# Performance work log

Hardware: AMD Instinct MI355X
Metric: run time of the kernel (lower is better)

## Reference

```python
import jax, jax.numpy as jnp
import numpy as np

N, C, H, W = 128, 3, 256, 256
MAXNORM = 5.371920351148152
MAX_SQ = 16  # static bound for data-dependent squaring loop
PADE_B = [6.476475253248e+16, 3.238237626624e+16, 7771770303897600.0,
          1187353796428800.0, 129060195264000.0, 10559470521600.0,
          670442572800.0, 33522128640.0, 1323241920.0, 40840800.0,
          960960.0, 16380.0, 182.0, 1.0]


def pade13(A):
    b = PADE_B
    I = jnp.eye(A.shape[-1], dtype=A.dtype)
    A2 = A @ A
    A4 = A2 @ A2
    A6 = A4 @ A2
    U = A @ (A6 @ (b[13] * A6 + b[11] * A4 + b[9] * A2)
             + b[7] * A6 + b[5] * A4 + b[3] * A2 + b[1] * I)
    V = (A6 @ (b[12] * A6 + b[10] * A4 + b[8] * A2)
         + b[6] * A6 + b[4] * A4 + b[2] * A2 + b[0] * I)
    return U, V


def expm_affine(theta):  # theta: [N,2,3] -> exp of padded 3x3, top 2 rows
    n = theta.shape[0]
    A = jnp.concatenate([theta, jnp.zeros((n, 1, 3), theta.dtype)], axis=1)
    fro = jnp.sqrt(jnp.sum(A * A, axis=(1, 2), keepdims=True))
    n_sq = jnp.maximum(0.0, jnp.ceil(jnp.log2(fro / MAXNORM)))
    Asc = A / (2.0 ** n_sq)
    U, V = pade13(Asc)
    R = jnp.linalg.solve(U + V, -U + V)
    k = n_sq.reshape(n).astype(jnp.int32)
    def body(i, Rc):
        return jnp.where((i < k)[:, None, None], jnp.matmul(Rc, Rc), Rc)
    R = jax.lax.fori_loop(0, MAX_SQ, body, R)
    return R[:, :2, :]


def affine_grid(theta, Ho, Wo):  # align_corners=True
    xs = jnp.linspace(-1.0, 1.0, Wo, dtype=theta.dtype)
    ys = jnp.linspace(-1.0, 1.0, Ho, dtype=theta.dtype)
    gy, gx = jnp.meshgrid(ys, xs, indexing='ij')          # [Ho,Wo]
    base = jnp.stack([gx, gy, jnp.ones_like(gx)], axis=-1)  # [Ho,Wo,3]
    return jnp.einsum('hwk,nck->nhwc', base, theta)        # [N,Ho,Wo,2]


def grid_sample(x, grid):  # bilinear, zeros padding, align_corners=True
    _, _, Hi, Wi = x.shape
    ix = (grid[..., 0] + 1.0) * 0.5 * (Wi - 1)
    iy = (grid[..., 1] + 1.0) * 0.5 * (Hi - 1)
    ix0 = jnp.floor(ix)
    iy0 = jnp.floor(iy)
    ix1 = ix0 + 1.0
    iy1 = iy0 + 1.0
    wx1 = ix - ix0; wx0 = 1.0 - wx1
    wy1 = iy - iy0; wy0 = 1.0 - wy1

    def gather(yy, xx):
        valid = ((yy >= 0) & (yy < Hi) & (xx >= 0) & (xx < Wi))
        yc = jnp.clip(yy, 0, Hi - 1).astype(jnp.int32)
        xc = jnp.clip(xx, 0, Wi - 1).astype(jnp.int32)
        vals = jax.vmap(lambda img, y, xi: img[:, y, xi])(x, yc, xc)  # [N,C,Ho,Wo]
        return vals * valid[:, None].astype(x.dtype)

    return (gather(iy0, ix0) * (wy0 * wx0)[:, None]
            + gather(iy0, ix1) * (wy0 * wx1)[:, None]
            + gather(iy1, ix0) * (wy1 * wx0)[:, None]
            + gather(iy1, ix1) * (wy1 * wx1)[:, None])


def setup_inputs() -> dict:
    key = jax.random.key(0)
    k1, k2 = jax.random.split(key)
    x = jax.random.normal(k1, (N, C, H, W), dtype=jnp.float32)
    theta = 0.1 * jax.random.normal(k2, (N, 6), dtype=jnp.float32)
    return {"x": x, "theta": theta}


def reference(x, theta):
    th = expm_affine(theta.reshape(-1, 2, 3))  # [N,2,3]
    grid = affine_grid(th, H, W)               # [N,H,W,2]
    return grid_sample(x, grid)                # [N,C,H,W]
```

## Files before the change

### kernel.cpp

```cpp
#include <hip/hip_runtime.h>

#define Ndim 128
#define Cdim 3
#define Hdim 256
#define Wdim 256
#define HW (Hdim * Wdim)
#define MAXNORM_F 5.371920351148152f

#define LCOLS 56
#define LROWS 48
#define LBUF  (LCOLS * LROWS)

typedef float vf2 __attribute__((ext_vector_type(2)));
typedef unsigned int uint32;

__device__ __forceinline__ void mm3f(const float a[3][3], const float b[3][3], float c[3][3]) {
    #pragma unroll
    for (int i = 0; i < 3; ++i)
        #pragma unroll
        for (int j = 0; j < 3; ++j) {
            float s = 0.0f;
            #pragma unroll
            for (int k = 0; k < 3; ++k) s = fmaf(a[i][k], b[k][j], s);
            c[i][j] = s;
        }
}

__global__ void expm_kernel(const float* __restrict__ theta, float* __restrict__ thOut) {
    int n = blockIdx.x * blockDim.x + threadIdx.x;
    if (n >= Ndim) return;

    const float b[14] = {6.476475253248e+16f, 3.238237626624e+16f, 7771770303897600.0f,
                         1187353796428800.0f, 129060195264000.0f, 10559470521600.0f,
                         670442572800.0f, 33522128640.0f, 1323241920.0f, 40840800.0f,
                         960960.0f, 16380.0f, 182.0f, 1.0f};

    float A[3][3];
    #pragma unroll
    for (int j = 0; j < 3; ++j) {
        A[0][j] = theta[n * 6 + j];
        A[1][j] = theta[n * 6 + 3 + j];
        A[2][j] = 0.0f;
    }

    float fro2 = 0.0f;
    #pragma unroll
    for (int i = 0; i < 3; ++i)
        #pragma unroll
        for (int j = 0; j < 3; ++j) fro2 = fmaf(A[i][j], A[i][j], fro2);
    float fro = sqrtf(fro2);

    float nsq = fmaxf(0.0f, ceilf(log2f(fro / MAXNORM_F)));
    int k = (int)nsq;
    float sc = exp2f(-nsq);
    #pragma unroll
    for (int i = 0; i < 3; ++i)
        #pragma unroll
        for (int j = 0; j < 3; ++j) A[i][j] *= sc;

    float A2[3][3], A4[3][3], A6[3][3], P[3][3], Wm[3][3], T[3][3], U[3][3], V[3][3];
    mm3f(A, A, A2);
    mm3f(A2, A2, A4);
    mm3f(A4, A2, A6);

    #pragma unroll
    for (int i = 0; i < 3; ++i)
        #pragma unroll
        for (int j = 0; j < 3; ++j)
            P[i][j] = b[13] * A6[i][j] + b[11] * A4[i][j] + b[9] * A2[i][j];
    mm3f(A6, P, T);
    #pragma unroll
    for (int i = 0; i < 3; ++i)
        #pragma unroll
        for (int j = 0; j < 3; ++j)
            Wm[i][j] = T[i][j] + b[7] * A6[i][j] + b[5] * A4[i][j] + b[3] * A2[i][j]
                       + (i == j ? b[1] : 0.0f);
    mm3f(A, Wm, U);

    #pragma unroll
    for (int i = 0; i < 3; ++i)
        #pragma unroll
        for (int j = 0; j < 3; ++j)
            P[i][j] = b[12] * A6[i][j] + b[10] * A4[i][j] + b[8] * A2[i][j];
    mm3f(A6, P, T);
    #pragma unroll
    for (int i = 0; i < 3; ++i)
        #pragma unroll
        for (int j = 0; j < 3; ++j)
            V[i][j] = T[i][j] + b[6] * A6[i][j] + b[4] * A4[i][j] + b[2] * A2[i][j]
                      + (i == j ? b[0] : 0.0f);

    float M[3][6];
    #pragma unroll
    for (int i = 0; i < 3; ++i)
        #pragma unroll
        for (int j = 0; j < 3; ++j) {
            M[i][j]     = U[i][j] + V[i][j];
            M[i][j + 3] = V[i][j] - U[i][j];
        }
    #pragma unroll
    for (int col = 0; col < 3; ++col) {
        int piv = col;
        float best = fabsf(M[col][col]);
        for (int r = col + 1; r < 3; ++r) {
            float v = fabsf(M[r][col]);
            if (v > best) { best = v; piv = r; }
        }
        if (piv != col) {
            #pragma unroll
            for (int j = 0; j < 6; ++j) {
                float t = M[col][j]; M[col][j] = M[piv][j]; M[piv][j] = t;
            }
        }
        float inv = 1.0f / M[col][col];
        #pragma unroll
        for (int j = 0; j < 6; ++j) M[col][j] *= inv;
        #pragma unroll
        for (int r = 0; r < 3; ++r) {
            if (r == col) continue;
            float f = M[r][col];
            #pragma unroll
            for (int j = 0; j < 6; ++j) M[r][j] -= f * M[col][j];
        }
    }
    float R[3][3];
    #pragma unroll
    for (int i = 0; i < 3; ++i)
        #pragma unroll
        for (int j = 0; j < 3; ++j) R[i][j] = M[i][j + 3];

    for (int i = 0; i < 16; ++i) {
        if (i < k) {
            float Rn[3][3];
            mm3f(R, R, Rn);
            #pragma unroll
            for (int a = 0; a < 3; ++a)
                #pragma unroll
                for (int c = 0; c < 3; ++c) R[a][c] = Rn[a][c];
        }
    }

    #pragma unroll
    for (int j = 0; j < 3; ++j) {
        thOut[n * 6 + j]     = (float)R[0][j];
        thOut[n * 6 + 3 + j] = (float)R[1][j];
    }
}

__global__ __launch_bounds__(256) void sample_kernel(const float* __restrict__ x,
                                                     const float* __restrict__ th,
                                                     float* __restrict__ out) {
    __shared__ float lds[2][LBUF];

    const int nwg_per_xcd = 8192 / 8;
    int bid = blockIdx.x;
    int wgid = (bid & 7) * nwg_per_xcd + (bid >> 3);

    int tw  = wgid & 7;
    int thp = (wgid >> 3) & 7;
    int n   = wgid >> 6;

    int tid = threadIdx.x;
    int w  = (tw << 5) + (tid & 31);
    int h0 = (thp << 5) + ((tid >> 5) << 2);

    const float* t = th + n * 6;
    float t0 = t[0], t1 = t[1], t2 = t[2], t3 = t[3], t4 = t[4], t5 = t[5];

    float Cx = 127.5f * (t2 - t0 - t1 + 1.0f);
    float Cy = 127.5f * (t5 - t3 - t4 + 1.0f);

    float fwA = (float)(tw << 5),  fwB = fwA + 31.0f;
    float fhA = (float)(thp << 5), fhB = fhA + 31.0f;
    float xlo = fminf(fwA * t0, fwB * t0) + fminf(fhA * t1, fhB * t1) + Cx;
    float xhi = fmaxf(fwA * t0, fwB * t0) + fmaxf(fhA * t1, fhB * t1) + Cx;
    float ylo = fminf(fwA * t3, fwB * t3) + fminf(fhA * t4, fhB * t4) + Cy;
    float yhi = fmaxf(fwA * t3, fwB * t3) + fmaxf(fhA * t4, fhB * t4) + Cy;
    int Xlo = (int)floorf(xlo) - 1, Xhi = (int)floorf(xhi) + 2;
    int Ylo = (int)floorf(ylo) - 1, Yhi = (int)floorf(yhi) + 2;
    int cn = Xhi - Xlo + 1;
    int rn = Yhi - Ylo + 1;

    size_t nbase = (size_t)n * Cdim * HW;

    float ixs[4], iys[4];
    float ixb = fmaf((float)w, t0, fmaf((float)h0, t1, Cx));
    float iyb = fmaf((float)w, t3, fmaf((float)h0, t4, Cy));
    #pragma unroll
    for (int p = 0; p < 4; ++p) {
        ixs[p] = fmaf((float)p, t1, ixb);
        iys[p] = fmaf((float)p, t4, iyb);
    }

    bool fast = (cn <= 52) && (rn <= LROWS) && (rn >= 1) && (cn >= 1);

    if (fast) {
        int bxw = (min(max(Xlo, 0), Wdim - LCOLS)) & ~3;
        int byw = min(max(Ylo, 0), Hdim - rn);
        int totc = 14 * rn;
        const float* gbase = x + nbase;

        auto stage = [&](int ch, int buf) {
            #pragma unroll
            for (int it = 0; it < 3; ++it) {
                int k = (it << 8) + tid;
                if (k < totc) {
                    int row = k / 14;
                    int col = k - row * 14;
                    const float* gp = gbase + (size_t)ch * HW
                                    + ((byw + row) << 8) + bxw + (col << 2);
                    __builtin_amdgcn_global_load_lds(
                        (const __attribute__((address_space(1))) uint32*)gp,
                        (__attribute__((address_space(3))) uint32*)
                            ((uint32*)&lds[buf][0] + ((size_t)k << 2)),
                        16, 0, 0);
                }
            }
        };

        bool interior = (Xlo >= 0) && (Xhi <= Wdim - 1) && (Ylo >= 0) && (Yhi <= Hdim - 1);

        stage(0, 0);

        int   basev[4];
        float wx1v[4], wy1v[4];
        if (interior) {
            #pragma unroll
            for (int p = 0; p < 4; ++p) {
                float ix = ixs[p], iy = iys[p];
                float fx = floorf(ix), fy = floorf(iy);
                wx1v[p] = ix - fx;
                wy1v[p] = iy - fy;
                basev[p] = ((int)fy - byw) * LCOLS + ((int)fx - bxw);
            }
        }
        size_t p0 = (size_t)h0 * Wdim + w;

        auto sample_interior = [&](int buf, int c) {
            float* o = out + nbase + (size_t)c * HW + p0;
            #pragma unroll
            for (int p = 0; p < 4; ++p) {
                const float* bp = &lds[buf][basev[p]];
                float v00 = bp[0],     v01 = bp[1];
                float v10 = bp[LCOLS], v11 = bp[LCOLS + 1];
                float wx1 = wx1v[p], wx0 = 1.0f - wx1;
                float wy1 = wy1v[p], wy0 = 1.0f - wy1;
                float top = fmaf(v01, wx1, v00 * wx0);
                float bot = fmaf(v11, wx1, v10 * wx0);
                __builtin_nontemporal_store(fmaf(wy1, bot, wy0 * top),
                                            o + (size_t)p * Wdim);
            }
        };

        auto sample_edge = [&](int buf, int c) {
            float* o = out + nbase + (size_t)c * HW + p0;
            #pragma unroll
            for (int p = 0; p < 4; ++p) {
                float ix = ixs[p], iy = iys[p];
                float fx = floorf(ix), fy = floorf(iy);
                int x0i = (int)fx, y0i = (int)fy;
                float wx1 = ix - fx, wx0 = 1.0f - wx1;
                float wy1 = iy - fy, wy0 = 1.0f - wy1;
                float mx0 = ((unsigned)x0i       < (unsigned)Wdim) ? 1.0f : 0.0f;
                float mx1 = ((unsigned)(x0i + 1) < (unsigned)Wdim) ? 1.0f : 0.0f;
                float my0 = ((unsigned)y0i       < (unsigned)Hdim) ? 1.0f : 0.0f;
                float my1 = ((unsigned)(y0i + 1) < (unsigned)Hdim) ? 1.0f : 0.0f;
                float wxm0 = wx0 * mx0, wxm1 = wx1 * mx1;
                float wym0 = wy0 * my0, wym1 = wy1 * my1;

                int lx0 = min(max(x0i - bxw, 0), LCOLS - 1);
                int lx1 = min(max(x0i + 1 - bxw, 0), LCOLS - 1);
                int ly0 = min(max(y0i - byw, 0), rn - 1);
                int ly1 = min(max(y0i + 1 - byw, 0), rn - 1);
                const float* B = &lds[buf][0];
                float v00 = B[ly0 * LCOLS + lx0], v01 = B[ly0 * LCOLS + lx1];
                float v10 = B[ly1 * LCOLS + lx0], v11 = B[ly1 * LCOLS + lx1];
                float top = fmaf(v01, wxm1, v00 * wxm0);
                float bot = fmaf(v11, wxm1, v10 * wxm0);
                __builtin_nontemporal_store(fmaf(wym1, bot, wym0 * top),
                                            o + (size_t)p * Wdim);
            }
        };

        __syncthreads();
        stage(1, 1);
        if (interior) sample_interior(0, 0); else sample_edge(0, 0);
        __syncthreads();
        stage(2, 0);
        if (interior) sample_interior(1, 1); else sample_edge(1, 1);
        __syncthreads();
        if (interior) sample_interior(0, 2); else sample_edge(0, 2);
    } else {
        const float* img0 = x + nbase;
        #pragma unroll
        for (int p = 0; p < 4; ++p) {
            float ix = ixs[p], iy = iys[p];
            float fx = floorf(ix), fy = floorf(iy);
            int ix0 = (int)fx, iy0 = (int)fy;
            float wx1 = ix - fx, wx0 = 1.0f - wx1;
            float wy1 = iy - fy, wy0 = 1.0f - wy1;
            float mx0 = ((unsigned)ix0       < (unsigned)Wdim) ? 1.0f : 0.0f;
            float mx1 = ((unsigned)(ix0 + 1) < (unsigned)Wdim) ? 1.0f : 0.0f;
            float my0 = ((unsigned)iy0       < (unsigned)Hdim) ? 1.0f : 0.0f;
            float my1 = ((unsigned)(iy0 + 1) < (unsigned)Hdim) ? 1.0f : 0.0f;
            int xc0 = min(max(ix0, 0), Wdim - 1);
            int xc1 = min(max(ix0 + 1, 0), Wdim - 1);
            int yc0 = min(max(iy0, 0), Hdim - 1);
            int yc1 = min(max(iy0 + 1, 0), Hdim - 1);
            float w00 = wy0 * wx0 * my0 * mx0;
            float w01 = wy0 * wx1 * my0 * mx1;
            float w10 = wy1 * wx0 * my1 * mx0;
            float w11 = wy1 * wx1 * my1 * mx1;
            int o00 = yc0 * Wdim + xc0, o01 = yc0 * Wdim + xc1;
            int o10 = yc1 * Wdim + xc0, o11 = yc1 * Wdim + xc1;
            #pragma unroll
            for (int c = 0; c < Cdim; ++c) {
                const float* img = img0 + (size_t)c * HW;
                float r = fmaf(img[o00], w00, fmaf(img[o01], w01,
                          fmaf(img[o10], w10, img[o11] * w11)));
                out[nbase + (size_t)c * HW + (size_t)(h0 + p) * Wdim + w] = r;
            }
        }
    }
}

extern "C" void kernel_launch(void* const* d_in, const int* in_sizes, int n_in,
                              void* d_out, int out_size, void* d_ws, size_t ws_size,
                              hipStream_t stream) {
    const float* x     = (const float*)d_in[0];
    const float* theta = (const float*)d_in[1];
    float* out = (float*)d_out;
    float* th  = (float*)d_ws;

    expm_kernel<<<1, 128, 0, stream>>>(theta, th);

    int nblocks = 8192;
    sample_kernel<<<nblocks, 256, 0, stream>>>(x, th, out);
}
```

Baseline: 41.30 us.

## Fuse matrix exponential into sampling kernel, drop separate expm launch

Removes the separate single-block expm kernel and has thread 0 of every sampling workgroup compute the 3x3 Pade matrix exponential for its batch item, sharing the result through LDS after a barrier. This eliminates one kernel launch and the dependency gap between the two kernels. In exchange, each of the 8192 workgroups redundantly runs the serial expm on one thread while the other threads wait at the barrier. It also precomputes the 1-minus interpolation weights once per pixel instead of once per channel.

```diff
diff --git a/kernel.cpp b/kernel.cpp
--- a/kernel.cpp
+++ b/kernel.cpp
@@ -26,10 +26,7 @@
         }
 }
 
-__global__ void expm_kernel(const float* __restrict__ theta, float* __restrict__ thOut) {
-    int n = blockIdx.x * blockDim.x + threadIdx.x;
-    if (n >= Ndim) return;
-
+__device__ void expm_affine_1thread(const float* __restrict__ theta, float* __restrict__ outR) {
     const float b[14] = {6.476475253248e+16f, 3.238237626624e+16f, 7771770303897600.0f,
                          1187353796428800.0f, 129060195264000.0f, 10559470521600.0f,
                          670442572800.0f, 33522128640.0f, 1323241920.0f, 40840800.0f,
@@ -38,8 +35,8 @@
     float A[3][3];
     #pragma unroll
     for (int j = 0; j < 3; ++j) {
-        A[0][j] = theta[n * 6 + j];
-        A[1][j] = theta[n * 6 + 3 + j];
+        A[0][j] = theta[j];
+        A[1][j] = theta[3 + j];
         A[2][j] = 0.0f;
     }
 
@@ -129,28 +126,27 @@
         #pragma unroll
         for (int j = 0; j < 3; ++j) R[i][j] = M[i][j + 3];
 
-    for (int i = 0; i < 16; ++i) {
-        if (i < k) {
-            float Rn[3][3];
-            mm3f(R, R, Rn);
-            #pragma unroll
-            for (int a = 0; a < 3; ++a)
-                #pragma unroll
-                for (int c = 0; c < 3; ++c) R[a][c] = Rn[a][c];
-        }
+    for (int i = 0; i < k; ++i) {
+        float Rn[3][3];
+        mm3f(R, R, Rn);
+        #pragma unroll
+        for (int a = 0; a < 3; ++a)
+            #pragma unroll
+            for (int c = 0; c < 3; ++c) R[a][c] = Rn[a][c];
     }
 
     #pragma unroll
     for (int j = 0; j < 3; ++j) {
-        thOut[n * 6 + j]     = (float)R[0][j];
-        thOut[n * 6 + 3 + j] = (float)R[1][j];
+        outR[j]     = R[0][j];
+        outR[3 + j] = R[1][j];
     }
 }
 
 __global__ __launch_bounds__(256) void sample_kernel(const float* __restrict__ x,
-                                                     const float* __restrict__ th,
+                                                     const float* __restrict__ theta,
                                                      float* __restrict__ out) {
     __shared__ float lds[2][LBUF];
+    __shared__ float thS[6];
 
     const int nwg_per_xcd = 8192 / 8;
     int bid = blockIdx.x;
@@ -164,8 +160,10 @@
     int w  = (tw << 5) + (tid & 31);
     int h0 = (thp << 5) + ((tid >> 5) << 2);
 
-    const float* t = th + n * 6;
-    float t0 = t[0], t1 = t[1], t2 = t[2], t3 = t[3], t4 = t[4], t5 = t[5];
+    if (tid == 0) expm_affine_1thread(theta + n * 6, thS);
+    __syncthreads();
+
+    float t0 = thS[0], t1 = thS[1], t2 = thS[2], t3 = thS[3], t4 = thS[4], t5 = thS[5];
 
     float Cx = 127.5f * (t2 - t0 - t1 + 1.0f);
     float Cy = 127.5f * (t5 - t3 - t4 + 1.0f);
@@ -223,14 +221,14 @@
         stage(0, 0);
 
         int   basev[4];
-        float wx1v[4], wy1v[4];
+        float wx1v[4], wx0v[4], wy1v[4], wy0v[4];
         if (interior) {
             #pragma unroll
             for (int p = 0; p < 4; ++p) {
                 float ix = ixs[p], iy = iys[p];
                 float fx = floorf(ix), fy = floorf(iy);
-                wx1v[p] = ix - fx;
-                wy1v[p] = iy - fy;
+                wx1v[p] = ix - fx; wx0v[p] = 1.0f - wx1v[p];
+                wy1v[p] = iy - fy; wy0v[p] = 1.0f - wy1v[p];
                 basev[p] = ((int)fy - byw) * LCOLS + ((int)fx - bxw);
             }
         }
@@ -243,11 +241,9 @@
                 const float* bp = &lds[buf][basev[p]];
                 float v00 = bp[0],     v01 = bp[1];
                 float v10 = bp[LCOLS], v11 = bp[LCOLS + 1];
-                float wx1 = wx1v[p], wx0 = 1.0f - wx1;
-                float wy1 = wy1v[p], wy0 = 1.0f - wy1;
-                float top = fmaf(v01, wx1, v00 * wx0);
-                float bot = fmaf(v11, wx1, v10 * wx0);
-                __builtin_nontemporal_store(fmaf(wy1, bot, wy0 * top),
+                float top = fmaf(v01, wx1v[p], v00 * wx0v[p]);
+                float bot = fmaf(v11, wx1v[p], v10 * wx0v[p]);
+                __builtin_nontemporal_store(fmaf(wy1v[p], bot, wy0v[p] * top),
                                             o + (size_t)p * Wdim);
             }
         };
@@ -330,10 +326,6 @@
     const float* x     = (const float*)d_in[0];
     const float* theta = (const float*)d_in[1];
     float* out = (float*)d_out;
-    float* th  = (float*)d_ws;
-
-    expm_kernel<<<1, 128, 0, stream>>>(theta, th);
-
-    int nblocks = 8192;
-    sample_kernel<<<nblocks, 256, 0, stream>>>(x, th, out);
+
+    sample_kernel<<<8192, 256, 0, stream>>>(x, theta, out);
 }
```

After: 44.27 us. 7.2% more time.
